# Kernel tuning notes

Measured on AMD Instinct MI355X. Metric: run time of the kernel, lower is better.

## Reference

```python
import jax, jax.numpy as jnp
import numpy as np

TEMPERATURE = 30.0


def _adaptive_pool_28(sk):
    # sk: [b, 1, H, W] with H, W divisible by 28 -> [b, 1, 28, 28]
    b, c, h, w = sk.shape
    fh, fw = h // 28, w // 28
    return sk.reshape(b, c, 28, fh, 28, fw).mean(axis=(3, 5))


def setup_inputs() -> dict:
    key = jax.random.key(0)
    ks = jax.random.split(key, 6)
    bs, C, H, W, K = 8, 256, 64, 64, 16
    return {
        "x": jax.random.normal(ks[0], (bs, C, H, W), dtype=jnp.float32),
        "scene_knowledge": jax.random.normal(ks[1], (bs, 1, 56, 56), dtype=jnp.float32),
        "weight": jax.random.normal(ks[2], (K, C, C, 3, 3), dtype=jnp.float32) * 0.02,
        "bias": jax.random.normal(ks[3], (K, C), dtype=jnp.float32) * 0.02,
        "att_w1": jax.random.normal(ks[4], (196, 784), dtype=jnp.float32) * 0.05,
        "att_w2": jax.random.normal(ks[5], (16, 196), dtype=jnp.float32) * 0.05,
    }


def reference(x, scene_knowledge, weight, bias, att_w1, att_w2):
    bs, C, h, w = x.shape
    K = weight.shape[0]

    # ---- Attention: pooled scene knowledge -> softmax over K experts ----
    pooled = _adaptive_pool_28(scene_knowledge).reshape(bs, 28 * 28)  # [bs, 784]
    hdn = jax.nn.relu(pooled @ att_w1.T)                               # [bs, 196]
    logits = hdn @ att_w2.T                                            # [bs, K]
    att = jax.nn.softmax(logits / TEMPERATURE, axis=-1)                # [bs, K]

    # ---- Aggregate per-sample conv weights and biases ----
    agg_w = jnp.einsum("bk,koihw->boihw", att, weight)  # [bs, C, C, 3, 3]
    agg_b = att @ bias                                   # [bs, C]

    # ---- Per-sample conv (equivalent to groups=bs trick in torch) ----
    def per_sample_conv(xi, wi):
        # xi: [C, h, w], wi: [C, C, 3, 3]
        return jax.lax.conv_general_dilated(
            xi[None], wi, window_strides=(1, 1), padding="SAME",
            dimension_numbers=("NCHW", "OIHW", "NCHW"))[0]

    out = jax.vmap(per_sample_conv)(x, agg_w)            # [bs, C, h, w]
    out = out + agg_b[:, :, None, None] + x              # bias + residual
    return out
```

## Files before the change

### kernel.cpp

```cpp
#include <hip/hip_runtime.h>
#include <stdint.h>
#include <stddef.h>

typedef __bf16 bf16;
typedef __bf16 bf16x8 __attribute__((ext_vector_type(8)));
typedef __bf16 bf16x4 __attribute__((ext_vector_type(4)));
typedef float f32x4 __attribute__((ext_vector_type(4)));

static_assert(sizeof(bf16x8) == 16, "bf16x8 must be 16B");

__device__ __forceinline__ void gload_lds16(const void* g, void* l) {
    __builtin_amdgcn_global_load_lds(
        (const __attribute__((address_space(1))) uint32_t*)g,
        (__attribute__((address_space(3))) uint32_t*)l, 16, 0, 0);
}

__global__ void attn_kernel(const float* __restrict__ sk,
                            const float* __restrict__ w1,
                            const float* __restrict__ w2,
                            float* __restrict__ att) {
    const int b = blockIdx.x, t = threadIdx.x;
    __shared__ float pooled[784];
    __shared__ float hdn[196];
    __shared__ float logits[16];
    const float* skb = sk + (size_t)b * 3136;
    for (int e = t; e < 784; e += 256) {
        int oy = e / 28, ox = e % 28;
        const float* p = skb + (oy * 2) * 56 + ox * 2;
        pooled[e] = 0.25f * (p[0] + p[1] + p[56] + p[57]);
    }
    __syncthreads();
    if (t < 196) {
        float s = 0.f;
        const float* wr = w1 + (size_t)t * 784;
        for (int i = 0; i < 784; ++i) s += pooled[i] * wr[i];
        hdn[t] = s > 0.f ? s : 0.f;
    }
    __syncthreads();
    if (t < 16) {
        float s = 0.f;
        const float* wr = w2 + (size_t)t * 196;
        for (int j = 0; j < 196; ++j) s += hdn[j] * wr[j];
        logits[t] = s * (1.0f / 30.0f);
    }
    __syncthreads();
    if (t == 0) {
        float m = logits[0];
        for (int k = 1; k < 16; ++k) m = fmaxf(m, logits[k]);
        float e16[16], sum = 0.f;
        for (int k = 0; k < 16; ++k) { e16[k] = expf(logits[k] - m); sum += e16[k]; }
        float inv = 1.f / sum;
        for (int k = 0; k < 16; ++k) att[b * 16 + k] = e16[k] * inv;
    }
}

__global__ __launch_bounds__(256) void agg_kernel(
    const float* __restrict__ weight,
    const float* __restrict__ bias,
    const float* __restrict__ att,
    bf16* __restrict__ aggw,
    float* __restrict__ aggb) {
    const int bid = blockIdx.x;
    const int co = bid & 255, chunk = bid >> 8;
    const int t = threadIdx.x;

    __shared__ bf16 accW[8 * 576];

    if (chunk == 0 && t < 8) {
        float s = 0.f;
        for (int k = 0; k < 16; ++k) s += att[t * 16 + k] * bias[k * 256 + co];
        aggb[t * 256 + co] = s;
    }

    if (t < 144) {
        const float* wbase = weight + (size_t)co * 2304 + (size_t)chunk * 576 + (size_t)t * 4;
        float4 wv[16];
#pragma unroll
        for (int k = 0; k < 16; ++k)
            wv[k] = *(const float4*)(wbase + (size_t)k * 589824);
        float a[8][4];
#pragma unroll
        for (int b = 0; b < 8; ++b)
#pragma unroll
            for (int j = 0; j < 4; ++j) a[b][j] = 0.f;
#pragma unroll
        for (int k = 0; k < 16; ++k) {
#pragma unroll
            for (int b = 0; b < 8; ++b) {
                const float av = att[b * 16 + k];
                a[b][0] += av * wv[k].x;
                a[b][1] += av * wv[k].y;
                a[b][2] += av * wv[k].z;
                a[b][3] += av * wv[k].w;
            }
        }
#pragma unroll
        for (int b = 0; b < 8; ++b) {
            bf16x4 v;
#pragma unroll
            for (int j = 0; j < 4; ++j) v[j] = (bf16)a[b][j];
            *(bf16x4*)&accW[b * 576 + t * 4] = v;
        }
    }
    __syncthreads();

    const int half = co >> 7, co_l = co & 127;
    for (int s = t; s < 576; s += 256) {
        const int b = s / 72, r = s - b * 72;
        const int pos = r >> 3, cg = r & 7;
        bf16x8 v;
#pragma unroll
        for (int c = 0; c < 8; ++c) v[c] = accW[b * 576 + (cg * 8 + c) * 9 + pos];
        size_t o = (((((size_t)b * 9 + pos) * 4 + chunk) * 2 + half) * 8 + cg) * 128 + co_l;
        *(bf16x8*)(aggw + o * 8) = v;
    }
}

__global__ void transpose_kernel(const float* __restrict__ x, bf16* __restrict__ xt) {
    const int bid = blockIdx.x;
    const int b = bid >> 6, y = bid & 63;
    const int t = threadIdx.x;
    __shared__ bf16 T[256 * 64];
    const float* src = x + (size_t)b * 256 * 4096 + (size_t)y * 64;
    for (int i = 0; i < 16; ++i) {
        int v = t + 256 * i;
        int ci = v >> 4, x4 = (v & 15) * 4;
        float4 f = *(const float4*)(src + (size_t)ci * 4096 + x4);
        bf16* d = &T[ci * 64 + x4];
        d[0] = (bf16)f.x; d[1] = (bf16)f.y; d[2] = (bf16)f.z; d[3] = (bf16)f.w;
    }
    __syncthreads();
    bf16* dstb = xt + (size_t)bid * 16384;
    for (int i = 0; i < 8; ++i) {
        int c2 = t + 256 * i;
        int cg = c2 >> 6, xx = c2 & 63;
        bf16x8 v;
#pragma unroll
        for (int c = 0; c < 8; ++c) v[c] = T[(cg * 8 + c) * 64 + xx];
        *(bf16x8*)(dstb + (size_t)c2 * 8) = v;
    }
}

__global__ __launch_bounds__(256, 2) void conv_kernel(
    const bf16* __restrict__ xt, const bf16* __restrict__ aggw,
    const float* __restrict__ aggb, const float* __restrict__ xin,
    float* __restrict__ out) {
    const int bid = blockIdx.x;
    const int ytile = bid & 31;
    const int half = (bid >> 5) & 1;
    const int b = bid >> 6;
    const int tid = threadIdx.x;
    const int wave = tid >> 6, lane = tid & 63;
    const int wm = wave & 1, wn = wave >> 1;
    const int lane15 = lane & 15, quad = lane >> 4;

    __shared__ __align__(16) bf16 Xs[4][8][66][8];
    __shared__ __align__(16) bf16 Ws[8][128][8];

    f32x4 acc[4][4];
#pragma unroll
    for (int mt = 0; mt < 4; ++mt)
#pragma unroll
        for (int nt = 0; nt < 4; ++nt) acc[mt][nt] = f32x4{0.f, 0.f, 0.f, 0.f};

    {
        uint4 z; z.x = z.y = z.z = z.w = 0u;
        uint4* p = (uint4*)&Xs[0][0][0][0];
        for (int i = tid; i < 2112; i += 256) p[i] = z;
    }

    const int yrow = ytile * 2 - 1 + wave;
    const bool rowok = (yrow >= 0) && (yrow < 64);
    const bf16* xsrc = xt + ((size_t)b * 64 + (rowok ? yrow : 0)) * 16384 + (size_t)lane * 8;
    bf16* xdstbase = &Xs[wave][0][1][0];

    for (int chunk = 0; chunk < 4; ++chunk) {
        __syncthreads();
        if (rowok) {
            const bf16* s0 = xsrc + (size_t)chunk * 4096;
#pragma unroll
            for (int cg = 0; cg < 8; ++cg)
                gload_lds16(s0 + cg * 512, xdstbase + cg * 528);
        }
        const bf16* wchunkbase = aggw + (((size_t)b * 36 + chunk) * 2 + half) * 8192;
        for (int pos = 0; pos < 9; ++pos) {
            if (pos) __syncthreads();
            const bf16* wsrc = wchunkbase + (size_t)pos * 65536 + wave * 2048 + (size_t)lane * 8;
            bf16* wdst = ((bf16*)Ws) + wave * 2048;
#pragma unroll
            for (int i = 0; i < 4; ++i)
                gload_lds16(wsrc + i * 512, wdst + i * 512);
            __syncthreads();
            const int kh = pos / 3, kw = pos - kh * 3;
            const int xr = wn + kh;
#pragma unroll
            for (int s = 0; s < 2; ++s) {
                const int cg = s * 4 + quad;
                bf16x8 afr[4], bfr[4];
#pragma unroll
                for (int mt = 0; mt < 4; ++mt)
                    afr[mt] = *(const bf16x8*)&Ws[cg][wm * 64 + mt * 16 + lane15][0];
#pragma unroll
                for (int nt = 0; nt < 4; ++nt)
                    bfr[nt] = *(const bf16x8*)&Xs[xr][cg][kw + nt * 16 + lane15][0];
#pragma unroll
                for (int mt = 0; mt < 4; ++mt)
#pragma unroll
                    for (int nt = 0; nt < 4; ++nt)
                        acc[mt][nt] = __builtin_amdgcn_mfma_f32_16x16x32_bf16(
                            afr[mt], bfr[nt], acc[mt][nt], 0, 0, 0);
            }
        }
    }

    const int y = ytile * 2 + wn;
#pragma unroll
    for (int mt = 0; mt < 4; ++mt) {
#pragma unroll
        for (int r = 0; r < 4; ++r) {
            const int co = half * 128 + wm * 64 + mt * 16 + quad * 4 + r;
            const float bbv = aggb[b * 256 + co];
            const size_t rowbase = (((size_t)b * 256 + co) * 64 + y) * 64;
#pragma unroll
            for (int nt = 0; nt < 4; ++nt) {
                const size_t oidx = rowbase + nt * 16 + lane15;
                out[oidx] = acc[mt][nt][r] + bbv + xin[oidx];
            }
        }
    }
}

extern "C" void kernel_launch(void* const* d_in, const int* in_sizes, int n_in,
                              void* d_out, int out_size, void* d_ws, size_t ws_size,
                              hipStream_t stream) {
    const float* x    = (const float*)d_in[0];
    const float* sk   = (const float*)d_in[1];
    const float* wgt  = (const float*)d_in[2];
    const float* bias = (const float*)d_in[3];
    const float* w1   = (const float*)d_in[4];
    const float* w2   = (const float*)d_in[5];
    float* out = (float*)d_out;

    char* ws = (char*)d_ws;
    float* att  = (float*)(ws + 0);
    float* aggb = (float*)(ws + 1024);
    bf16*  aggw = (bf16*)(ws + 16384);
    bf16*  xt   = (bf16*)(ws + 16384 + 9437184);

    attn_kernel<<<8, 256, 0, stream>>>(sk, w1, w2, att);
    agg_kernel<<<1024, 256, 0, stream>>>(wgt, bias, att, aggw, aggb);
    transpose_kernel<<<512, 256, 0, stream>>>(x, xt);
    conv_kernel<<<512, 256, 0, stream>>>(xt, aggw, aggb, x, out);
}
```

Measured before the change: 190.2 us.

## Double-buffer input tiles in LDS and load weight fragments directly from global

The conv kernel now double-buffers the input-row tile in shared memory, prefetching the next channel chunk while computing the current one. Weight fragments are read straight from global memory into registers for each tap, which removes the per-tap weight staging through LDS and the two barriers around it. The cost is doubled input LDS and global-latency weight loads on the MFMA critical path, relying on L1/L2 caching and unrolling to hide that latency. Register pressure also grows from unrolling the nine taps.

```diff
diff --git a/kernel.cpp b/kernel.cpp
--- a/kernel.cpp
+++ b/kernel.cpp
@@ -154,8 +154,7 @@
     const int wm = wave & 1, wn = wave >> 1;
     const int lane15 = lane & 15, quad = lane >> 4;
 
-    __shared__ __align__(16) bf16 Xs[4][8][66][8];
-    __shared__ __align__(16) bf16 Ws[8][128][8];
+    __shared__ __align__(16) bf16 Xs[2][4][8][66][8];
 
     f32x4 acc[4][4];
 #pragma unroll
@@ -165,52 +164,63 @@
 
     {
         uint4 z; z.x = z.y = z.z = z.w = 0u;
-        uint4* p = (uint4*)&Xs[0][0][0][0];
-        for (int i = tid; i < 2112; i += 256) p[i] = z;
+        uint4* p = (uint4*)&Xs[0][0][0][0][0];
+        for (int i = tid; i < 4224; i += 256) p[i] = z;
     }
 
     const int yrow = ytile * 2 - 1 + wave;
     const bool rowok = (yrow >= 0) && (yrow < 64);
     const bf16* xsrc = xt + ((size_t)b * 64 + (rowok ? yrow : 0)) * 16384 + (size_t)lane * 8;
-    bf16* xdstbase = &Xs[wave][0][1][0];
+
+    const bf16* wlane = aggw + (size_t)b * 9 * 65536 + (size_t)half * 8192
+                      + (size_t)quad * 1024 + (size_t)(wm * 64 + lane15) * 8;
+
+    __syncthreads();
+    if (rowok) {
+        bf16* xdst = &Xs[0][wave][0][1][0];
+#pragma unroll
+        for (int cg = 0; cg < 8; ++cg)
+            gload_lds16(xsrc + cg * 512, xdst + cg * 528);
+    }
+    __syncthreads();
 
     for (int chunk = 0; chunk < 4; ++chunk) {
-        __syncthreads();
-        if (rowok) {
-            const bf16* s0 = xsrc + (size_t)chunk * 4096;
+        const int cur = chunk & 1;
+        if (chunk < 3 && rowok) {
+            const bf16* s0 = xsrc + (size_t)(chunk + 1) * 4096;
+            bf16* xdst = &Xs[cur ^ 1][wave][0][1][0];
 #pragma unroll
             for (int cg = 0; cg < 8; ++cg)
-                gload_lds16(s0 + cg * 512, xdstbase + cg * 528);
-        }
-        const bf16* wchunkbase = aggw + (((size_t)b * 36 + chunk) * 2 + half) * 8192;
+                gload_lds16(s0 + cg * 512, xdst + cg * 528);
+        }
+        const bf16* wchunk = wlane + (size_t)chunk * 16384;
+#pragma unroll
         for (int pos = 0; pos < 9; ++pos) {
-            if (pos) __syncthreads();
-            const bf16* wsrc = wchunkbase + (size_t)pos * 65536 + wave * 2048 + (size_t)lane * 8;
-            bf16* wdst = ((bf16*)Ws) + wave * 2048;
-#pragma unroll
-            for (int i = 0; i < 4; ++i)
-                gload_lds16(wsrc + i * 512, wdst + i * 512);
-            __syncthreads();
             const int kh = pos / 3, kw = pos - kh * 3;
             const int xr = wn + kh;
+            const bf16* wtap = wchunk + (size_t)pos * 65536;
+            bf16x8 afr[2][4];
+#pragma unroll
+            for (int s = 0; s < 2; ++s)
+#pragma unroll
+                for (int mt = 0; mt < 4; ++mt)
+                    afr[s][mt] = *(const bf16x8*)(wtap + s * 4096 + mt * 128);
 #pragma unroll
             for (int s = 0; s < 2; ++s) {
                 const int cg = s * 4 + quad;
-                bf16x8 afr[4], bfr[4];
-#pragma unroll
-                for (int mt = 0; mt < 4; ++mt)
-                    afr[mt] = *(const bf16x8*)&Ws[cg][wm * 64 + mt * 16 + lane15][0];
+                bf16x8 bfr[4];
 #pragma unroll
                 for (int nt = 0; nt < 4; ++nt)
-                    bfr[nt] = *(const bf16x8*)&Xs[xr][cg][kw + nt * 16 + lane15][0];
+                    bfr[nt] = *(const bf16x8*)&Xs[cur][xr][cg][kw + nt * 16 + lane15][0];
 #pragma unroll
                 for (int mt = 0; mt < 4; ++mt)
 #pragma unroll
                     for (int nt = 0; nt < 4; ++nt)
                         acc[mt][nt] = __builtin_amdgcn_mfma_f32_16x16x32_bf16(
-                            afr[mt], bfr[nt], acc[mt][nt], 0, 0, 0);
+                            afr[s][mt], bfr[nt], acc[mt][nt], 0, 0, 0);
             }
         }
+        __syncthreads();
     }
 
     const int y = ytile * 2 + wn;
```

Result: slower. 208.1 us (+9.4%).

## Double-buffer per-position weight tiles in LDS to overlap loads with MFMA

Applied to the files above, without the earlier changes.

Doubles the weight staging buffer in shared memory. The kernel now prefetches the next kernel-position (or the next chunk's first position) weight slice into the alternate buffer while MFMAs run on the current one, with a single wait and barrier per step instead of two barriers around a blocking load. The input-row chunk load is still issued between chunks, after the compute. This hides global-to-LDS latency for the weights, at the cost of roughly 16KB more LDS per block and a slightly more complex barrier schedule.

```diff
diff --git a/kernel.cpp b/kernel.cpp
--- a/kernel.cpp
+++ b/kernel.cpp
@@ -155,7 +155,7 @@
     const int lane15 = lane & 15, quad = lane >> 4;
 
     __shared__ __align__(16) bf16 Xs[4][8][66][8];
-    __shared__ __align__(16) bf16 Ws[8][128][8];
+    __shared__ __align__(16) bf16 Ws[2][8][128][8];
 
     f32x4 acc[4][4];
 #pragma unroll
@@ -168,38 +168,56 @@
         uint4* p = (uint4*)&Xs[0][0][0][0];
         for (int i = tid; i < 2112; i += 256) p[i] = z;
     }
+    __syncthreads();
 
     const int yrow = ytile * 2 - 1 + wave;
     const bool rowok = (yrow >= 0) && (yrow < 64);
     const bf16* xsrc = xt + ((size_t)b * 64 + (rowok ? yrow : 0)) * 16384 + (size_t)lane * 8;
     bf16* xdstbase = &Xs[wave][0][1][0];
 
+    const bf16* wsrcbase = aggw + (size_t)b * 589824 + (size_t)half * 8192
+                         + (size_t)wave * 2048 + (size_t)lane * 8;
+    bf16* wslice0 = ((bf16*)&Ws[0][0][0][0]) + wave * 2048;
+    bf16* wslice1 = ((bf16*)&Ws[1][0][0][0]) + wave * 2048;
+
+    if (rowok) {
+#pragma unroll
+        for (int cg = 0; cg < 8; ++cg)
+            gload_lds16(xsrc + cg * 512, xdstbase + cg * 528);
+    }
+#pragma unroll
+    for (int i = 0; i < 4; ++i)
+        gload_lds16(wsrcbase + i * 512, wslice0 + i * 512);
+    asm volatile("s_waitcnt vmcnt(0)" ::: "memory");
+    __builtin_amdgcn_s_barrier();
+
     for (int chunk = 0; chunk < 4; ++chunk) {
-        __syncthreads();
-        if (rowok) {
-            const bf16* s0 = xsrc + (size_t)chunk * 4096;
-#pragma unroll
-            for (int cg = 0; cg < 8; ++cg)
-                gload_lds16(s0 + cg * 512, xdstbase + cg * 528);
-        }
-        const bf16* wchunkbase = aggw + (((size_t)b * 36 + chunk) * 2 + half) * 8192;
+#pragma unroll
         for (int pos = 0; pos < 9; ++pos) {
-            if (pos) __syncthreads();
-            const bf16* wsrc = wchunkbase + (size_t)pos * 65536 + wave * 2048 + (size_t)lane * 8;
-            bf16* wdst = ((bf16*)Ws) + wave * 2048;
-#pragma unroll
-            for (int i = 0; i < 4; ++i)
-                gload_lds16(wsrc + i * 512, wdst + i * 512);
-            __syncthreads();
+            const int bufp = (chunk + pos) & 1;
+            bf16* wnext = bufp ? wslice0 : wslice1;
+            if (pos < 8) {
+                const bf16* s0 = wsrcbase + (size_t)(pos + 1) * 65536 + (size_t)chunk * 16384;
+#pragma unroll
+                for (int i = 0; i < 4; ++i)
+                    gload_lds16(s0 + i * 512, wnext + i * 512);
+            } else if (chunk < 3) {
+                const bf16* s0 = wsrcbase + (size_t)(chunk + 1) * 16384;
+#pragma unroll
+                for (int i = 0; i < 4; ++i)
+                    gload_lds16(s0 + i * 512, wnext + i * 512);
+            }
             const int kh = pos / 3, kw = pos - kh * 3;
             const int xr = wn + kh;
+            const bf16* wcur = (const bf16*)&Ws[bufp][0][0][0];
 #pragma unroll
             for (int s = 0; s < 2; ++s) {
                 const int cg = s * 4 + quad;
                 bf16x8 afr[4], bfr[4];
 #pragma unroll
                 for (int mt = 0; mt < 4; ++mt)
-                    afr[mt] = *(const bf16x8*)&Ws[cg][wm * 64 + mt * 16 + lane15][0];
+                    afr[mt] = *(const bf16x8*)(wcur + (size_t)cg * 1024
+                                               + (size_t)(wm * 64 + mt * 16 + lane15) * 8);
 #pragma unroll
                 for (int nt = 0; nt < 4; ++nt)
                     bfr[nt] = *(const bf16x8*)&Xs[xr][cg][kw + nt * 16 + lane15][0];
@@ -210,6 +228,20 @@
                         acc[mt][nt] = __builtin_amdgcn_mfma_f32_16x16x32_bf16(
                             afr[mt], bfr[nt], acc[mt][nt], 0, 0, 0);
             }
+            if (chunk < 3 || pos < 8) {
+                asm volatile("s_waitcnt vmcnt(0) lgkmcnt(0)" ::: "memory");
+                __builtin_amdgcn_s_barrier();
+            }
+        }
+        if (chunk < 3) {
+            if (rowok) {
+                const bf16* s0 = xsrc + (size_t)(chunk + 1) * 4096;
+#pragma unroll
+                for (int cg = 0; cg < 8; ++cg)
+                    gload_lds16(s0 + cg * 512, xdstbase + cg * 528);
+            }
+            asm volatile("s_waitcnt vmcnt(0)" ::: "memory");
+            __builtin_amdgcn_s_barrier();
         }
     }
 
```

Measured after the change: 199.1 us. 4.7% more time.

## Fuse weight aggregation with input transpose and parallelize attention MLP

Applied to the files above, without the earlier changes.

Merges the agg and transpose kernels into one launch, with separate block ranges for each job, so one kernel boundary disappears and the two memory-bound phases can overlap. The aggregation now has each block handle 8 output channels, which gives wider contiguous stores into aggw. The attention kernel runs 1024 threads and splits each dot product across 16 lanes with shuffle reductions instead of running one serial loop per thread. The conv block-index mapping changes so consecutive blocks take different batch/half slices of the same y tile, which alters L2 locality. The fused kernel uses about 74KB of LDS per block, which may lower occupancy.

```diff
diff --git a/kernel.cpp b/kernel.cpp
--- a/kernel.cpp
+++ b/kernel.cpp
@@ -5,6 +5,7 @@
 typedef __bf16 bf16;
 typedef __bf16 bf16x8 __attribute__((ext_vector_type(8)));
 typedef __bf16 bf16x4 __attribute__((ext_vector_type(4)));
+typedef __bf16 bf16x2 __attribute__((ext_vector_type(2)));
 typedef float f32x4 __attribute__((ext_vector_type(4)));
 
 static_assert(sizeof(bf16x8) == 16, "bf16x8 must be 16B");
@@ -15,33 +16,47 @@
         (__attribute__((address_space(3))) uint32_t*)l, 16, 0, 0);
 }
 
-__global__ void attn_kernel(const float* __restrict__ sk,
-                            const float* __restrict__ w1,
-                            const float* __restrict__ w2,
-                            float* __restrict__ att) {
+__global__ __launch_bounds__(1024) void attn_kernel(const float* __restrict__ sk,
+                                                    const float* __restrict__ w1,
+                                                    const float* __restrict__ w2,
+                                                    float* __restrict__ att) {
     const int b = blockIdx.x, t = threadIdx.x;
     __shared__ float pooled[784];
     __shared__ float hdn[196];
     __shared__ float logits[16];
     const float* skb = sk + (size_t)b * 3136;
-    for (int e = t; e < 784; e += 256) {
-        int oy = e / 28, ox = e % 28;
+    if (t < 784) {
+        int oy = t / 28, ox = t % 28;
         const float* p = skb + (oy * 2) * 56 + ox * 2;
-        pooled[e] = 0.25f * (p[0] + p[1] + p[56] + p[57]);
-    }
-    __syncthreads();
-    if (t < 196) {
+        pooled[t] = 0.25f * (p[0] + p[1] + p[56] + p[57]);
+    }
+    __syncthreads();
+    const int q = t & 15, jg = t >> 4;
+#pragma unroll
+    for (int rep = 0; rep < 4; ++rep) {
+        const int j = rep * 64 + jg;
         float s = 0.f;
-        const float* wr = w1 + (size_t)t * 784;
-        for (int i = 0; i < 784; ++i) s += pooled[i] * wr[i];
-        hdn[t] = s > 0.f ? s : 0.f;
-    }
-    __syncthreads();
-    if (t < 16) {
+        if (j < 196) {
+            const float* wr = w1 + (size_t)j * 784 + q;
+#pragma unroll 7
+            for (int i = 0; i < 49; ++i) s += pooled[q + i * 16] * wr[i * 16];
+        }
+#pragma unroll
+        for (int off = 8; off; off >>= 1) s += __shfl_xor(s, off, 16);
+        if (j < 196 && q == 0) hdn[j] = s > 0.f ? s : 0.f;
+    }
+    __syncthreads();
+    if (t < 256) {
+        const int jj = t >> 4, qq = t & 15;
         float s = 0.f;
-        const float* wr = w2 + (size_t)t * 196;
-        for (int j = 0; j < 196; ++j) s += hdn[j] * wr[j];
-        logits[t] = s * (1.0f / 30.0f);
+#pragma unroll
+        for (int i = 0; i < 13; ++i) {
+            const int idx = qq + i * 16;
+            if (idx < 196) s += hdn[idx] * w2[jj * 196 + idx];
+        }
+#pragma unroll
+        for (int off = 8; off; off >>= 1) s += __shfl_xor(s, off, 16);
+        if (qq == 0) logits[jj] = s * (1.0f / 30.0f);
     }
     __syncthreads();
     if (t == 0) {
@@ -54,35 +69,66 @@
     }
 }
 
-__global__ __launch_bounds__(256) void agg_kernel(
+__global__ __launch_bounds__(256) void aggt_kernel(
     const float* __restrict__ weight,
     const float* __restrict__ bias,
     const float* __restrict__ att,
     bf16* __restrict__ aggw,
-    float* __restrict__ aggb) {
-    const int bid = blockIdx.x;
-    const int co = bid & 255, chunk = bid >> 8;
+    float* __restrict__ aggb,
+    const float* __restrict__ x,
+    bf16* __restrict__ xt) {
+    __shared__ __align__(16) char smem[73984];
     const int t = threadIdx.x;
 
-    __shared__ bf16 accW[8 * 576];
-
-    if (chunk == 0 && t < 8) {
+    if (blockIdx.x >= 128) {
+        const int bid = blockIdx.x - 128;
+        const int b = bid >> 6, y = bid & 63;
+        bf16* T = (bf16*)smem;
+        const float* src = x + (size_t)b * 256 * 4096 + (size_t)y * 64;
+        for (int i = 0; i < 16; ++i) {
+            int v = t + 256 * i;
+            int ci = v >> 4, x4 = (v & 15) * 4;
+            float4 f = *(const float4*)(src + (size_t)ci * 4096 + x4);
+            bf16* d = &T[ci * 64 + x4];
+            d[0] = (bf16)f.x; d[1] = (bf16)f.y; d[2] = (bf16)f.z; d[3] = (bf16)f.w;
+        }
+        __syncthreads();
+        bf16* dstb = xt + (size_t)bid * 16384;
+        for (int i = 0; i < 8; ++i) {
+            int c2 = t + 256 * i;
+            int cg = c2 >> 6, xx = c2 & 63;
+            bf16x8 v;
+#pragma unroll
+            for (int c = 0; c < 8; ++c) v[c] = T[(cg * 8 + c) * 64 + xx];
+            *(bf16x8*)(dstb + (size_t)c2 * 8) = v;
+        }
+        return;
+    }
+
+    const int chunk = blockIdx.x >> 5, cog = blockIdx.x & 31;
+    const int half = cog >> 4;
+    bf16* accW = (bf16*)smem;
+
+    if (chunk == 0 && t < 64) {
+        const int b = t >> 3, co = cog * 8 + (t & 7);
         float s = 0.f;
-        for (int k = 0; k < 16; ++k) s += att[t * 16 + k] * bias[k * 256 + co];
-        aggb[t * 256 + co] = s;
-    }
-
-    if (t < 144) {
-        const float* wbase = weight + (size_t)co * 2304 + (size_t)chunk * 576 + (size_t)t * 4;
-        float4 wv[16];
+        for (int k = 0; k < 16; ++k) s += att[b * 16 + k] * bias[k * 256 + co];
+        aggb[b * 256 + co] = s;
+    }
+
+#pragma unroll
+    for (int r = 0; r < 9; ++r) {
+        const int id = t + 256 * r;
+        const int co_i = id / 288, e2 = id - co_i * 288;
+        const int co = cog * 8 + co_i;
+        const float* wbase = weight + (size_t)co * 2304 + (size_t)chunk * 576 + 2 * e2;
+        float2 wv[16];
 #pragma unroll
         for (int k = 0; k < 16; ++k)
-            wv[k] = *(const float4*)(wbase + (size_t)k * 589824);
-        float a[8][4];
-#pragma unroll
-        for (int b = 0; b < 8; ++b)
-#pragma unroll
-            for (int j = 0; j < 4; ++j) a[b][j] = 0.f;
+            wv[k] = *(const float2*)(wbase + (size_t)k * 589824);
+        float a[8][2];
+#pragma unroll
+        for (int b = 0; b < 8; ++b) { a[b][0] = 0.f; a[b][1] = 0.f; }
 #pragma unroll
         for (int k = 0; k < 16; ++k) {
 #pragma unroll
@@ -90,54 +136,29 @@
                 const float av = att[b * 16 + k];
                 a[b][0] += av * wv[k].x;
                 a[b][1] += av * wv[k].y;
-                a[b][2] += av * wv[k].z;
-                a[b][3] += av * wv[k].w;
             }
         }
 #pragma unroll
         for (int b = 0; b < 8; ++b) {
-            bf16x4 v;
-#pragma unroll
-            for (int j = 0; j < 4; ++j) v[j] = (bf16)a[b][j];
-            *(bf16x4*)&accW[b * 576 + t * 4] = v;
-        }
-    }
-    __syncthreads();
-
-    const int half = co >> 7, co_l = co & 127;
-    for (int s = t; s < 576; s += 256) {
-        const int b = s / 72, r = s - b * 72;
+            bf16x2 v; v[0] = (bf16)a[b][0]; v[1] = (bf16)a[b][1];
+            *(bf16x2*)&accW[(co_i * 8 + b) * 578 + 2 * e2] = v;
+        }
+    }
+    __syncthreads();
+
+    const int cogl = cog & 15;
+#pragma unroll
+    for (int i = 0; i < 18; ++i) {
+        const int s = t + 256 * i;
+        const int piece = s >> 3, sub = s & 7;
+        const int b = piece / 72, r = piece - b * 72;
         const int pos = r >> 3, cg = r & 7;
         bf16x8 v;
 #pragma unroll
-        for (int c = 0; c < 8; ++c) v[c] = accW[b * 576 + (cg * 8 + c) * 9 + pos];
-        size_t o = (((((size_t)b * 9 + pos) * 4 + chunk) * 2 + half) * 8 + cg) * 128 + co_l;
-        *(bf16x8*)(aggw + o * 8) = v;
-    }
-}
-
-__global__ void transpose_kernel(const float* __restrict__ x, bf16* __restrict__ xt) {
-    const int bid = blockIdx.x;
-    const int b = bid >> 6, y = bid & 63;
-    const int t = threadIdx.x;
-    __shared__ bf16 T[256 * 64];
-    const float* src = x + (size_t)b * 256 * 4096 + (size_t)y * 64;
-    for (int i = 0; i < 16; ++i) {
-        int v = t + 256 * i;
-        int ci = v >> 4, x4 = (v & 15) * 4;
-        float4 f = *(const float4*)(src + (size_t)ci * 4096 + x4);
-        bf16* d = &T[ci * 64 + x4];
-        d[0] = (bf16)f.x; d[1] = (bf16)f.y; d[2] = (bf16)f.z; d[3] = (bf16)f.w;
-    }
-    __syncthreads();
-    bf16* dstb = xt + (size_t)bid * 16384;
-    for (int i = 0; i < 8; ++i) {
-        int c2 = t + 256 * i;
-        int cg = c2 >> 6, xx = c2 & 63;
-        bf16x8 v;
-#pragma unroll
-        for (int c = 0; c < 8; ++c) v[c] = T[(cg * 8 + c) * 64 + xx];
-        *(bf16x8*)(dstb + (size_t)c2 * 8) = v;
+        for (int c = 0; c < 8; ++c)
+            v[c] = accW[(sub * 8 + b) * 578 + (cg * 8 + c) * 9 + pos];
+        const size_t G = ((((size_t)b * 9 + pos) * 4 + chunk) * 2 + half) * 8 + cg;
+        *(bf16x8*)(aggw + G * 1024 + cogl * 64 + sub * 8) = v;
     }
 }
 
@@ -146,9 +167,8 @@
     const float* __restrict__ aggb, const float* __restrict__ xin,
     float* __restrict__ out) {
     const int bid = blockIdx.x;
-    const int ytile = bid & 31;
-    const int half = (bid >> 5) & 1;
-    const int b = bid >> 6;
+    const int slice = bid & 15, ytile = bid >> 4;
+    const int b = slice >> 1, half = slice & 1;
     const int tid = threadIdx.x;
     const int wave = tid >> 6, lane = tid & 63;
     const int wm = wave & 1, wn = wave >> 1;
@@ -247,8 +267,7 @@
     bf16*  aggw = (bf16*)(ws + 16384);
     bf16*  xt   = (bf16*)(ws + 16384 + 9437184);
 
-    attn_kernel<<<8, 256, 0, stream>>>(sk, w1, w2, att);
-    agg_kernel<<<1024, 256, 0, stream>>>(wgt, bias, att, aggw, aggb);
-    transpose_kernel<<<512, 256, 0, stream>>>(x, xt);
+    attn_kernel<<<8, 1024, 0, stream>>>(sk, w1, w2, att);
+    aggt_kernel<<<640, 256, 0, stream>>>(wgt, bias, att, aggw, aggb, x, xt);
     conv_kernel<<<512, 256, 0, stream>>>(xt, aggw, aggb, x, out);
 }
```

After: 178.8 us. 6.0% less time.
